# Kernel optimization log

Hardware: AMD Instinct MI355X
Metric: run time of the kernel (lower is better)

The kernel has to match this reference:

```python
import jax, jax.numpy as jnp
import numpy as np

N_A = 50000
N_B = 50000
E = 500000
D = 128


def setup_inputs() -> dict:
    key = jax.random.key(0)
    ks = jax.random.split(key, 16)
    s = 0.02
    inp = {
        "x_a": jax.random.normal(ks[0], (N_A, D), jnp.float32),
        "x_b": jax.random.normal(ks[1], (N_B, D), jnp.float32),
        # shared GraphEdgeWeight params
        "Wp": jax.random.normal(ks[2], (D, D), jnp.float32) * s,
        "bp": jnp.zeros((D,), jnp.float32),
        "Wc": jax.random.normal(ks[3], (D, D), jnp.float32) * s,
        "bc": jnp.zeros((D,), jnp.float32),
        "W1": jax.random.normal(ks[4], (D, 3 * D), jnp.float32) * s,
        "b1": jnp.zeros((D,), jnp.float32),
        "W2": jax.random.normal(ks[5], (1, D), jnp.float32) * s,
        "b2": jnp.zeros((1,), jnp.float32),
        # GraphConv params for edge type A->B
        "Wrel_ab": jax.random.normal(ks[6], (D, D), jnp.float32) * s,
        "brel_ab": jnp.zeros((D,), jnp.float32),
        "Wroot_ab": jax.random.normal(ks[7], (D, D), jnp.float32) * s,
        "broot_ab": jnp.zeros((D,), jnp.float32),
        # GraphConv params for edge type B->A
        "Wrel_ba": jax.random.normal(ks[8], (D, D), jnp.float32) * s,
        "brel_ba": jnp.zeros((D,), jnp.float32),
        "Wroot_ba": jax.random.normal(ks[9], (D, D), jnp.float32) * s,
        "broot_ba": jnp.zeros((D,), jnp.float32),
        # edge indices: row0 = src node ids, row1 = dst node ids
        "ei_ab": jax.random.randint(ks[10], (2, E), 0, N_A),
        "ei_ba": jax.random.randint(ks[11], (2, E), 0, N_B),
    }
    return inp


def _edge_type_conv(x_src, x_dst, ei, Wp, bp, Wc, bc, W1, b1, W2, b2,
                    Wrel, brel, Wroot, broot, n_dst):
    # gather endpoint features per edge  [E, D]
    par = x_src[ei[0]]
    cld = x_dst[ei[1]]
    # GraphEdgeWeight: encoders (Linear + LeakyReLU; dropout inactive in eval)
    ep = jax.nn.leaky_relu(par @ Wp.T + bp, negative_slope=0.01)
    ec = jax.nn.leaky_relu(cld @ Wc.T + bc, negative_slope=0.01)
    feat = jnp.concatenate([ep, ec, jnp.abs(par - cld)], axis=-1)  # [E, 3D]
    h = jax.nn.relu(feat @ W1.T + b1)                              # [E, D]
    w = jax.nn.sigmoid(h @ W2.T + b2)[:, 0]                        # [E]
    # GraphConv: out_i = Wrel @ sum_{j->i} w_e x_j + Wroot @ x_i (+ biases)
    msg = jax.ops.segment_sum(par * w[:, None], ei[1], num_segments=n_dst)
    return msg @ Wrel.T + brel + x_dst @ Wroot.T + broot


def reference(x_a, x_b, Wp, bp, Wc, bc, W1, b1, W2, b2,
              Wrel_ab, brel_ab, Wroot_ab, broot_ab,
              Wrel_ba, brel_ba, Wroot_ba, broot_ba,
              ei_ab, ei_ba):
    out_b = _edge_type_conv(x_a, x_b, ei_ab, Wp, bp, Wc, bc, W1, b1, W2, b2,
                            Wrel_ab, brel_ab, Wroot_ab, broot_ab, N_B)
    out_a = _edge_type_conv(x_b, x_a, ei_ba, Wp, bp, Wc, bc, W1, b1, W2, b2,
                            Wrel_ba, brel_ba, Wroot_ba, broot_ba, N_A)
    return out_a, out_b
```

## Files before the change

kernel.cpp:

```cpp
#include <hip/hip_runtime.h>
#include <hip/hip_bf16.h>

typedef unsigned short u16;
typedef __attribute__((ext_vector_type(8))) short bf16x8;
typedef __attribute__((ext_vector_type(2))) short s16x2;
typedef __attribute__((ext_vector_type(4))) float f32x4;

#define N_NODES 50000
#define EDGES 500000
#define WPT 31250
#define NWAVES 3125
#define NBLK 782

__device__ __forceinline__ u16 f2bf(float f) {
  return __builtin_bit_cast(u16, __float2bfloat16(f));
}
__device__ __forceinline__ float bf2f(u16 u) {
  return __builtin_bit_cast(float, ((unsigned)u) << 16);
}
__device__ __forceinline__ float bfe(bf16x8 v, int j) {
  return bf2f((u16)v[j]);
}

__device__ __forceinline__ void pk_atomic_bf16(u16* addr, float lo, float hi) {
#if __has_builtin(__builtin_amdgcn_global_atomic_fadd_v2bf16)
  s16x2 v;
  v[0] = (short)f2bf(lo);
  v[1] = (short)f2bf(hi);
  __builtin_amdgcn_global_atomic_fadd_v2bf16(
      (__attribute__((address_space(1))) s16x2*)addr, v);
#else
  unsigned* p = (unsigned*)addr;
  unsigned old = *p, assumed;
  do {
    assumed = old;
    float l2 = bf2f((u16)(assumed & 0xffff)) + lo;
    float h2 = bf2f((u16)(assumed >> 16)) + hi;
    unsigned nv = (unsigned)f2bf(l2) | ((unsigned)f2bf(h2) << 16);
    old = atomicCAS(p, assumed, nv);
  } while (old != assumed);
#endif
}

__global__ __launch_bounds__(256) void prep_weights_zero(
    const float* __restrict__ Wp, const float* __restrict__ Wc,
    const float* __restrict__ W1,
    const float* __restrict__ Wrel_ab, const float* __restrict__ Wroot_ab,
    const float* __restrict__ Wrel_ba, const float* __restrict__ Wroot_ba,
    u16* __restrict__ out, u16* __restrict__ msg)
{
  if (blockIdx.x >= 576) {
    size_t t = (size_t)(blockIdx.x - 576) * 256 + threadIdx.x;
    bf16x8 z = {0, 0, 0, 0, 0, 0, 0, 0};
    *(bf16x8*)(msg + t * 8) = z;
    return;
  }
  int tid = blockIdx.x * 256 + threadIdx.x;
  int m = tid >> 14;
  int idx = tid & 16383;
  int r = idx >> 7;
  int c = idx & 127;
  float val;
  switch (m) {
    case 0: val = Wp[r * 128 + c]; break;
    case 1: val = Wc[r * 128 + c]; break;
    case 2: val = W1[r * 384 + c]; break;
    case 3: val = W1[r * 384 + 128 + c]; break;
    case 4: val = W1[r * 384 + 256 + c]; break;
    case 5: val = Wrel_ab[r * 128 + c]; break;
    case 6: val = Wroot_ab[r * 128 + c]; break;
    case 7: val = Wrel_ba[r * 128 + c]; break;
    default: val = Wroot_ba[r * 128 + c]; break;
  }
  out[tid] = f2bf(val);
}

__global__ __launch_bounds__(256) void encoder2(
    const float* __restrict__ xa, const float* __restrict__ xb,
    const u16* __restrict__ Wp_b, const float* __restrict__ bp,
    const u16* __restrict__ Wc_b, const float* __restrict__ bc,
    const u16* __restrict__ W1a_b, const float* __restrict__ b1,
    const u16* __restrict__ W1b_b,
    u16* __restrict__ xa_bf, u16* __restrict__ xb_bf,
    u16* __restrict__ u_a, u16* __restrict__ v_a,
    u16* __restrict__ u_b, u16* __restrict__ v_b)
{
  __shared__ u16 tile[4][2176];
  int widx = threadIdx.x >> 6;
  int w = blockIdx.x * 4 + widx;
  int type = (w >= NBLK * 4) ? 1 : 0;
  int nw = w - type * NBLK * 4;
  if (nw >= NWAVES) nw = NWAVES - 1;
  const float* x = type ? xb : xa;
  u16* xbf_out = type ? xb_bf : xa_bf;
  u16* u_out = type ? u_b : u_a;
  u16* v_out = type ? v_b : v_a;
  int row0 = nw * 16;
  int lane = threadIdx.x & 63;
  int col = lane & 15;
  int quad = lane >> 4;
  u16* tl = tile[widx];

  bf16x8 af[4];
#pragma unroll
  for (int ks = 0; ks < 4; ks++) {
    const float* xp = x + (size_t)(row0 + col) * 128 + ks * 32 + quad * 8;
    f32x4 lo = *(const f32x4*)xp;
    f32x4 hi = *(const f32x4*)(xp + 4);
    bf16x8 o;
#pragma unroll
    for (int j = 0; j < 4; j++) {
      o[j]     = (short)f2bf(lo[j]);
      o[j + 4] = (short)f2bf(hi[j]);
    }
    af[ks] = o;
    *(bf16x8*)(xbf_out + (size_t)(row0 + col) * 128 + ks * 32 + quad * 8) = o;
  }

  f32x4 zero = {0.f, 0.f, 0.f, 0.f};

  for (int chain = 0; chain < 2; chain++) {
    const u16* Wenc = chain ? Wc_b : Wp_b;
    const float* benc = chain ? bc : bp;
    const u16* Wmix = chain ? W1b_b : W1a_b;
    const float* bmix = chain ? nullptr : b1;
    u16* outp = chain ? v_out : u_out;

    f32x4 acc[8];
#pragma unroll
    for (int nt = 0; nt < 8; nt++) acc[nt] = zero;
#pragma unroll
    for (int ks = 0; ks < 4; ks++) {
      const u16* wp = Wenc + col * 128 + ks * 32 + quad * 8;
#pragma unroll
      for (int nt = 0; nt < 8; nt++) {
        bf16x8 bf = *(const bf16x8*)(wp + nt * 2048);
        acc[nt] = __builtin_amdgcn_mfma_f32_16x16x32_bf16(af[ks], bf, acc[nt], 0, 0, 0);
      }
    }
#pragma unroll
    for (int nt = 0; nt < 8; nt++) {
      float be = benc[nt * 16 + col];
#pragma unroll
      for (int r = 0; r < 4; r++) {
        float v = acc[nt][r] + be;
        v = v > 0.f ? v : 0.01f * v;
        tl[(quad * 4 + r) * 136 + nt * 16 + col] = f2bf(v);
      }
    }
    bf16x8 a2[4];
#pragma unroll
    for (int ks = 0; ks < 4; ks++)
      a2[ks] = *(const bf16x8*)&tl[col * 136 + ks * 32 + quad * 8];

    f32x4 acc2[8];
#pragma unroll
    for (int nt = 0; nt < 8; nt++) acc2[nt] = zero;
#pragma unroll
    for (int ks = 0; ks < 4; ks++) {
      const u16* wp = Wmix + col * 128 + ks * 32 + quad * 8;
#pragma unroll
      for (int nt = 0; nt < 8; nt++) {
        bf16x8 bf = *(const bf16x8*)(wp + nt * 2048);
        acc2[nt] = __builtin_amdgcn_mfma_f32_16x16x32_bf16(a2[ks], bf, acc2[nt], 0, 0, 0);
      }
    }
#pragma unroll
    for (int nt = 0; nt < 8; nt++) {
      float bm = bmix ? bmix[nt * 16 + col] : 0.f;
#pragma unroll
      for (int r = 0; r < 4; r++)
        outp[(size_t)(row0 + quad * 4 + r) * 128 + nt * 16 + col] = f2bf(acc2[nt][r] + bm);
    }
  }
}

__global__ __launch_bounds__(256) void out_gemm2(
    const u16* __restrict__ xa_bf, const u16* __restrict__ xb_bf,
    const u16* __restrict__ msgX_a, const u16* __restrict__ msgX_b,
    const u16* __restrict__ Wrelba_b, const u16* __restrict__ Wrelab_b,
    const u16* __restrict__ Wrootba_b, const u16* __restrict__ Wrootab_b,
    const float* __restrict__ brel_ba, const float* __restrict__ broot_ba,
    const float* __restrict__ brel_ab, const float* __restrict__ broot_ab,
    float* __restrict__ out_a, float* __restrict__ out_b)
{
  int w = blockIdx.x * 4 + (threadIdx.x >> 6);
  int type = (w >= NBLK * 4) ? 1 : 0;
  int nw = w - type * NBLK * 4;
  if (nw >= NWAVES) return;
  const u16* xbf = type ? xb_bf : xa_bf;
  const u16* msg = type ? msgX_b : msgX_a;
  const u16* Wrel = type ? Wrelab_b : Wrelba_b;
  const u16* Wroot = type ? Wrootab_b : Wrootba_b;
  const float* brel = type ? brel_ab : brel_ba;
  const float* broot = type ? broot_ab : broot_ba;
  float* outp = type ? out_b : out_a;
  int row0 = nw * 16;
  int lane = threadIdx.x & 63;
  int col = lane & 15;
  int quad = lane >> 4;

  bf16x8 ax[4], am[4];
#pragma unroll
  for (int ks = 0; ks < 4; ks++) {
    ax[ks] = *(const bf16x8*)(xbf + (size_t)(row0 + col) * 128 + ks * 32 + quad * 8);
    am[ks] = *(const bf16x8*)(msg + (size_t)(row0 + col) * 128 + ks * 32 + quad * 8);
  }

  f32x4 zero = {0.f, 0.f, 0.f, 0.f};
  f32x4 acc[8];
#pragma unroll
  for (int nt = 0; nt < 8; nt++) acc[nt] = zero;
#pragma unroll
  for (int ks = 0; ks < 4; ks++) {
    const u16* wp1 = Wrel + col * 128 + ks * 32 + quad * 8;
    const u16* wp2 = Wroot + col * 128 + ks * 32 + quad * 8;
#pragma unroll
    for (int nt = 0; nt < 8; nt++) {
      bf16x8 b1f = *(const bf16x8*)(wp1 + nt * 2048);
      acc[nt] = __builtin_amdgcn_mfma_f32_16x16x32_bf16(am[ks], b1f, acc[nt], 0, 0, 0);
      bf16x8 b2f = *(const bf16x8*)(wp2 + nt * 2048);
      acc[nt] = __builtin_amdgcn_mfma_f32_16x16x32_bf16(ax[ks], b2f, acc[nt], 0, 0, 0);
    }
  }
#pragma unroll
  for (int nt = 0; nt < 8; nt++) {
    int c = nt * 16 + col;
    float b = brel[c] + broot[c];
#pragma unroll
    for (int r = 0; r < 4; r++)
      outp[(size_t)(row0 + quad * 4 + r) * 128 + c] = acc[nt][r] + b;
  }
}

__global__ __launch_bounds__(256) void edge_fused(
    const u16* __restrict__ xa_bf, const u16* __restrict__ xb_bf,
    const int* __restrict__ ei_ab, const int* __restrict__ ei_ba,
    const u16* __restrict__ W1c,
    const u16* __restrict__ u_a, const u16* __restrict__ v_a,
    const u16* __restrict__ u_b, const u16* __restrict__ v_b,
    const float* __restrict__ W2, const float* __restrict__ b2p,
    u16* __restrict__ msgX_a, u16* __restrict__ msgX_b)
{
  __shared__ u16 tld[4][2176];
  int widx = threadIdx.x >> 6;
  int w = blockIdx.x * 4 + widx;
  int type = (w >= WPT) ? 1 : 0;
  int e0 = (w - type * WPT) * 16;
  const u16* xs = type ? xb_bf : xa_bf;
  const u16* xd = type ? xa_bf : xb_bf;
  const int* ei = type ? ei_ba : ei_ab;
  const u16* uT = type ? u_b : u_a;
  const u16* vT = type ? v_a : v_b;
  u16* msgX     = type ? msgX_a : msgX_b;

  int lane = threadIdx.x & 63;
  int col = lane & 15;
  int quad = lane >> 4;

  int em = e0 + col;
  int si = ei[em];
  int di = ei[EDGES + em];

  int e = e0 + (lane >> 2);
  int s2 = ei[e];
  int d2 = ei[EDGES + e];
  int c0 = (lane & 3) * 32;

  bf16x8 af[4];
  bf16x8 d8[4];
#pragma unroll
  for (int ks = 0; ks < 4; ks++) {
    af[ks] = *(const bf16x8*)(xs + (size_t)si * 128 + ks * 32 + quad * 8);
    d8[ks] = *(const bf16x8*)(xd + (size_t)di * 128 + ks * 32 + quad * 8);
  }

  const u16* urow = uT + (size_t)s2 * 128 + c0;
  const u16* vrow = vT + (size_t)d2 * 128 + c0;
  bf16x8 UU[4], VV[4];
#pragma unroll
  for (int k = 0; k < 4; k++) {
    UU[k] = *(const bf16x8*)(urow + k * 8);
    VV[k] = *(const bf16x8*)(vrow + k * 8);
  }

  f32x4 zero = {0.f, 0.f, 0.f, 0.f};
  f32x4 acc[8];
#pragma unroll
  for (int nt = 0; nt < 8; nt++) acc[nt] = zero;
#pragma unroll
  for (int ks = 0; ks < 4; ks++) {
    bf16x8 df;
#pragma unroll
    for (int j = 0; j < 8; j++)
      df[j] = (short)f2bf(__builtin_fabsf(bfe(af[ks], j) - bfe(d8[ks], j)));
    const u16* wp = W1c + col * 128 + ks * 32 + quad * 8;
#pragma unroll
    for (int nt = 0; nt < 8; nt++) {
      bf16x8 bf = *(const bf16x8*)(wp + nt * 2048);
      acc[nt] = __builtin_amdgcn_mfma_f32_16x16x32_bf16(df, bf, acc[nt], 0, 0, 0);
    }
  }

  u16* tl = tld[widx];
#pragma unroll
  for (int nt = 0; nt < 8; nt++)
#pragma unroll
    for (int r = 0; r < 4; r++)
      tl[(quad * 4 + r) * 136 + nt * 16 + col] = f2bf(acc[nt][r]);

  const u16* trow = &tl[(lane >> 2) * 136 + c0];
  float p = 0.f;
#pragma unroll
  for (int k = 0; k < 4; k++) {
    bf16x8 tt = *(const bf16x8*)(trow + k * 8);
    f32x4 w0 = *(const f32x4*)(W2 + c0 + k * 8);
    f32x4 w1 = *(const f32x4*)(W2 + c0 + k * 8 + 4);
#pragma unroll
    for (int j = 0; j < 4; j++) {
      float q0 = bfe(tt, j) + bfe(UU[k], j) + bfe(VV[k], j);
      if (q0 > 0.f) p += q0 * w0[j];
      float q1 = bfe(tt, j + 4) + bfe(UU[k], j + 4) + bfe(VV[k], j + 4);
      if (q1 > 0.f) p += q1 * w1[j];
    }
  }
  p += __shfl_xor(p, 1, 64);
  p += __shfl_xor(p, 2, 64);
  float wgt = 1.f / (1.f + __expf(-(p + b2p[0])));

#pragma unroll
  for (int ks = 0; ks < 4; ks++)
    *(bf16x8*)&tl[col * 136 + ks * 32 + quad * 8] = af[ks];

#pragma unroll
  for (int r = 0; r < 4; r++) {
    int src_lane = (quad * 4 + r) * 4;
    float wr = __shfl(wgt, src_lane, 64);
    int dr = __shfl(d2, src_lane, 64);
    u16* mrow = msgX + (size_t)dr * 128;
    const u16* xrow = &tl[(quad * 4 + r) * 136];
#pragma unroll
    for (int nt = 0; nt < 4; nt++) {
      int c = nt * 32 + col * 2;
      unsigned xv = *(const unsigned*)(xrow + c);
      pk_atomic_bf16(mrow + c, wr * bf2f((u16)(xv & 0xffff)),
                               wr * bf2f((u16)(xv >> 16)));
    }
  }
}

extern "C" void kernel_launch(void* const* d_in, const int* in_sizes, int n_in,
                              void* d_out, int out_size, void* d_ws, size_t ws_size,
                              hipStream_t stream) {
  const float* x_a      = (const float*)d_in[0];
  const float* x_b      = (const float*)d_in[1];
  const float* Wp       = (const float*)d_in[2];
  const float* bp       = (const float*)d_in[3];
  const float* Wc       = (const float*)d_in[4];
  const float* bc       = (const float*)d_in[5];
  const float* W1       = (const float*)d_in[6];
  const float* b1       = (const float*)d_in[7];
  const float* W2       = (const float*)d_in[8];
  const float* b2       = (const float*)d_in[9];
  const float* Wrel_ab  = (const float*)d_in[10];
  const float* brel_ab  = (const float*)d_in[11];
  const float* Wroot_ab = (const float*)d_in[12];
  const float* broot_ab = (const float*)d_in[13];
  const float* Wrel_ba  = (const float*)d_in[14];
  const float* brel_ba  = (const float*)d_in[15];
  const float* Wroot_ba = (const float*)d_in[16];
  const float* broot_ba = (const float*)d_in[17];
  const int*   ei_ab    = (const int*)d_in[18];
  const int*   ei_ba    = (const int*)d_in[19];

  char* ws = (char*)d_ws;
  u16* Wb        = (u16*)ws;
  u16* Wp_b      = Wb + 0 * 16384;
  u16* Wc_b      = Wb + 1 * 16384;
  u16* W1a_b     = Wb + 2 * 16384;
  u16* W1b_b     = Wb + 3 * 16384;
  u16* W1c_b     = Wb + 4 * 16384;
  u16* Wrelab_b  = Wb + 5 * 16384;
  u16* Wrootab_b = Wb + 6 * 16384;
  u16* Wrelba_b  = Wb + 7 * 16384;
  u16* Wrootba_b = Wb + 8 * 16384;

  u16* xa_bf   = (u16*)(ws + 1048576);
  u16* xb_bf   = (u16*)(ws + 13848576);
  u16* u_a     = (u16*)(ws + 26648576);
  u16* v_a     = (u16*)(ws + 39448576);
  u16* u_b     = (u16*)(ws + 52248576);
  u16* v_b     = (u16*)(ws + 65048576);
  u16* msgX_a  = (u16*)(ws + 77848576);
  u16* msgX_b  = (u16*)(ws + 90648576);

  float* out_a = (float*)d_out;
  float* out_b = out_a + (size_t)N_NODES * 128;

  prep_weights_zero<<<6826, 256, 0, stream>>>(Wp, Wc, W1, Wrel_ab, Wroot_ab,
                                              Wrel_ba, Wroot_ba, Wb, msgX_a);

  encoder2<<<2 * NBLK, 256, 0, stream>>>(x_a, x_b, Wp_b, bp, Wc_b, bc,
                                         W1a_b, b1, W1b_b,
                                         xa_bf, xb_bf, u_a, v_a, u_b, v_b);

  edge_fused<<<15625, 256, 0, stream>>>(xa_bf, xb_bf, ei_ab, ei_ba, W1c_b,
                                        u_a, v_a, u_b, v_b,
                                        W2, b2, msgX_a, msgX_b);

  out_gemm2<<<2 * NBLK, 256, 0, stream>>>(xa_bf, xb_bf, msgX_a, msgX_b,
                                          Wrelba_b, Wrelab_b,
                                          Wrootba_b, Wrootab_b,
                                          brel_ba, broot_ba, brel_ab, broot_ab,
                                          out_a, out_b);
}
```

Before: 697.9 us.

## Split edge kernel into weight computation and separate row-wise scatter kernel

Splits the fused edge kernel in two. The first kernel computes per-edge sigmoid weights and writes them to scratch space borrowed from the output buffer. A new scatter kernel then has each wave take 64 edges and issue one coalesced 256-byte packed bf16 atomic row per edge. This drops the LDS transpose and the scattered 4-row atomic pattern, and it frees the MFMA kernel from atomic latency. The cost is an extra launch and a second read of the edge indices and source rows, and it relies on out_gemm2 overwriting the borrowed output memory later.

```diff
diff --git a/kernel.cpp b/kernel.cpp
--- a/kernel.cpp
+++ b/kernel.cpp
@@ -9,6 +9,7 @@
 #define N_NODES 50000
 #define EDGES 500000
 #define WPT 31250
+#define SWPT 7813
 #define NWAVES 3125
 #define NBLK 782
 
@@ -233,14 +234,14 @@
   }
 }
 
-__global__ __launch_bounds__(256) void edge_fused(
+__global__ __launch_bounds__(256) void edge_w(
     const u16* __restrict__ xa_bf, const u16* __restrict__ xb_bf,
     const int* __restrict__ ei_ab, const int* __restrict__ ei_ba,
     const u16* __restrict__ W1c,
     const u16* __restrict__ u_a, const u16* __restrict__ v_a,
     const u16* __restrict__ u_b, const u16* __restrict__ v_b,
     const float* __restrict__ W2, const float* __restrict__ b2p,
-    u16* __restrict__ msgX_a, u16* __restrict__ msgX_b)
+    float* __restrict__ w_ab, float* __restrict__ w_ba)
 {
   __shared__ u16 tld[4][2176];
   int widx = threadIdx.x >> 6;
@@ -252,7 +253,7 @@
   const int* ei = type ? ei_ba : ei_ab;
   const u16* uT = type ? u_b : u_a;
   const u16* vT = type ? v_a : v_b;
-  u16* msgX     = type ? msgX_a : msgX_b;
+  float* wout   = type ? w_ba : w_ab;
 
   int lane = threadIdx.x & 63;
   int col = lane & 15;
@@ -328,23 +329,54 @@
   p += __shfl_xor(p, 2, 64);
   float wgt = 1.f / (1.f + __expf(-(p + b2p[0])));
 
-#pragma unroll
-  for (int ks = 0; ks < 4; ks++)
-    *(bf16x8*)&tl[col * 136 + ks * 32 + quad * 8] = af[ks];
-
-#pragma unroll
-  for (int r = 0; r < 4; r++) {
-    int src_lane = (quad * 4 + r) * 4;
-    float wr = __shfl(wgt, src_lane, 64);
-    int dr = __shfl(d2, src_lane, 64);
-    u16* mrow = msgX + (size_t)dr * 128;
-    const u16* xrow = &tl[(quad * 4 + r) * 136];
-#pragma unroll
-    for (int nt = 0; nt < 4; nt++) {
-      int c = nt * 32 + col * 2;
-      unsigned xv = *(const unsigned*)(xrow + c);
-      pk_atomic_bf16(mrow + c, wr * bf2f((u16)(xv & 0xffff)),
-                               wr * bf2f((u16)(xv >> 16)));
+  if ((lane & 3) == 0) wout[e] = wgt;
+}
+
+__global__ __launch_bounds__(256) void edge_scatter(
+    const u16* __restrict__ xa_bf, const u16* __restrict__ xb_bf,
+    const int* __restrict__ ei_ab, const int* __restrict__ ei_ba,
+    const float* __restrict__ w_ab, const float* __restrict__ w_ba,
+    u16* __restrict__ msgX_a, u16* __restrict__ msgX_b)
+{
+  int wv = blockIdx.x * 4 + (threadIdx.x >> 6);
+  int lane = threadIdx.x & 63;
+  int type = (wv >= SWPT) ? 1 : 0;
+  int lw = wv - type * SWPT;
+  if (lw >= SWPT) return;
+  int e0 = lw * 64;
+  if (e0 >= EDGES) return;
+  const u16* xs = type ? xb_bf : xa_bf;
+  const int* ei = type ? ei_ba : ei_ab;
+  const float* wE = type ? w_ba : w_ab;
+  u16* msgX = type ? msgX_a : msgX_b;
+
+  int eL = e0 + lane;
+  bool ok = eL < EDGES;
+  int sv = ok ? ei[eL] : 0;
+  int dv = ok ? ei[EDGES + eL] : 0;
+  float wl = ok ? wE[eL] : 0.f;
+
+  int nE = EDGES - e0;
+  if (nE >= 64) {
+#pragma unroll 8
+    for (int j = 0; j < 64; j++) {
+      float wr = __shfl(wl, j, 64);
+      int sr = __shfl(sv, j, 64);
+      int dr = __shfl(dv, j, 64);
+      unsigned xv = *(const unsigned*)(xs + (size_t)sr * 128 + lane * 2);
+      pk_atomic_bf16(msgX + (size_t)dr * 128 + lane * 2,
+                     wr * bf2f((u16)(xv & 0xffff)),
+                     wr * bf2f((u16)(xv >> 16)));
+    }
+  } else {
+    for (int j = 0; j < nE; j++) {
+      float wr = __shfl(wl, j, 64);
+      int sr = __shfl(sv, j, 64);
+      int dr = __shfl(dv, j, 64);
+      unsigned xv = *(const unsigned*)(xs + (size_t)sr * 128 + lane * 2);
+      pk_atomic_bf16(msgX + (size_t)dr * 128 + lane * 2,
+                     wr * bf2f((u16)(xv & 0xffff)),
+                     wr * bf2f((u16)(xv >> 16)));
     }
   }
 }
@@ -397,6 +429,9 @@
   float* out_a = (float*)d_out;
   float* out_b = out_a + (size_t)N_NODES * 128;
 
+  float* w_ab = (float*)d_out;
+  float* w_ba = w_ab + EDGES;
+
   prep_weights_zero<<<6826, 256, 0, stream>>>(Wp, Wc, W1, Wrel_ab, Wroot_ab,
                                               Wrel_ba, Wroot_ba, Wb, msgX_a);
 
@@ -404,9 +439,12 @@
                                          W1a_b, b1, W1b_b,
                                          xa_bf, xb_bf, u_a, v_a, u_b, v_b);
 
-  edge_fused<<<15625, 256, 0, stream>>>(xa_bf, xb_bf, ei_ab, ei_ba, W1c_b,
-                                        u_a, v_a, u_b, v_b,
-                                        W2, b2, msgX_a, msgX_b);
+  edge_w<<<15625, 256, 0, stream>>>(xa_bf, xb_bf, ei_ab, ei_ba, W1c_b,
+                                    u_a, v_a, u_b, v_b,
+                                    W2, b2, w_ab, w_ba);
+
+  edge_scatter<<<3907, 256, 0, stream>>>(xa_bf, xb_bf, ei_ab, ei_ba,
+                                         w_ab, w_ba, msgX_a, msgX_b);
 
   out_gemm2<<<2 * NBLK, 256, 0, stream>>>(xa_bf, xb_bf, msgX_a, msgX_b,
                                           Wrelba_b, Wrelab_b,
```

New measurement: 871.2 us. +24.8%, slower.
